# Optimization experiments

Measured on AMD Instinct MI355X. Metric: run time of the kernel, lower is better.

## Reference

```python
import jax, jax.numpy as jnp
import numpy as np

B, D, PRE, NXT, J, K, A = 1000, 8, 98, 2048, 32, 64, 5

def setup_inputs() -> dict:
    key = jax.random.key(0)
    ks = jax.random.split(key, 20)
    s = 0.05  # weight scale to keep activations sane
    inp = {
        'x': jax.random.normal(ks[0], (B, D * PRE), jnp.float32),
        'W1': jax.random.normal(ks[1], (D, NXT, PRE), jnp.float32) * s,
        'b1': jax.random.normal(ks[2], (D, NXT), jnp.float32) * s,
        'Wc': jax.random.normal(ks[3], (D, J, NXT), jnp.float32) * s,
        'bc': jax.random.normal(ks[4], (D, J), jnp.float32) * s,
        'cut_layer_bias': jax.random.normal(ks[5], (J,), jnp.float32) * s,
        'b_mat': jax.random.normal(ks[6], (D, J), jnp.float32) * s,
        'h_mat': jax.random.normal(ks[7], (D, K, A), jnp.float32),
        'a_mat': jax.random.normal(ks[8], (J, A), jnp.float32) * s,
        'noise': jax.random.normal(ks[9], (J, A), jnp.float32),  # tau2 = 1.0
        'W3': jax.random.normal(ks[10], (98, J), jnp.float32) * s,
        'b3': jax.random.normal(ks[11], (98,), jnp.float32) * s,
        'W4': jax.random.normal(ks[12], (49, 98), jnp.float32) * s,
        'b4': jax.random.normal(ks[13], (49,), jnp.float32) * s,
        'Wo': jax.random.normal(ks[14], (10, 49), jnp.float32) * s,
        'bo': jax.random.normal(ks[15], (10,), jnp.float32) * s,
    }
    # one-hot subcarrier allocation: each symbol j assigned exactly one subcarrier k
    assign = jax.random.randint(ks[16], (J,), 0, K)
    inp['indicator'] = jax.nn.one_hot(assign, K, dtype=jnp.float32)
    return inp


def reference(x, W1, b1, Wc, bc, cut_layer_bias, b_mat, h_mat, a_mat, indicator,
              noise, W3, b3, W4, b4, Wo, bo):
    b = x.shape[0]
    xs = x.reshape(b, D, PRE)                                   # split across devices
    sub = jax.nn.relu(jnp.einsum('bdi,doi->bdo', xs, W1) + b1)  # [B,D,NXT]
    # online cross-device mean/var via .item() in torch => stats are non-differentiable scalars
    m = jnp.mean(sub, axis=(0, 2))                              # per-device mean [D]
    v = jnp.mean((sub - m[None, :, None]) ** 2, axis=(0, 2))    # per-device var  [D]
    gm = jax.lax.stop_gradient(jnp.mean(m))
    gv = jax.lax.stop_gradient(jnp.mean(v))
    norm = (sub - gm) / jnp.sqrt(gv + 1e-6)
    dso = jnp.einsum('bdo,djo->bdj', norm, Wc) + bc             # device-side outputs [B,D,J]
    # channel: gather assigned subcarrier per symbol, combine with receive beamformers a_j
    h_sel = jnp.einsum('jk,nkd->njd', indicator, h_mat)         # [D,J,A]
    h_vec = jnp.einsum('njd,jd->nj', h_sel, a_mat)              # [D,J]
    received = jnp.einsum('bnj,nj->bj', dso * b_mat[None], h_vec)  # [B,J]
    received = received + jnp.sum(a_mat * noise, axis=1)[None, :]  # scaled noise per symbol
    h = jax.nn.relu(received + cut_layer_bias)
    h = jax.nn.relu(h @ W3.T + b3)
    h = jax.nn.relu(h @ W4.T + b4)
    return jax.nn.log_softmax(h @ Wo.T + bo, axis=1)
```

## Files before the change

kernel.cpp:

```cpp
#include <hip/hip_runtime.h>
#include <math.h>

#define B_ 1000
#define D_ 8
#define PRE_ 98
#define NXT_ 2048
#define J_ 32
#define K_ 64
#define A_ 5

typedef __attribute__((ext_vector_type(8))) __bf16 bf16x8;
typedef __attribute__((ext_vector_type(4))) float f32x4;
typedef __attribute__((ext_vector_type(16))) float f32x16;
typedef __attribute__((ext_vector_type(8))) unsigned short us8;

__device__ __forceinline__ unsigned cvtpk(float lo, float hi) {
  unsigned r;
  asm("v_cvt_pk_bf16_f32 %0, %1, %2" : "=v"(r) : "v"(lo), "v"(hi));
  return r;
}

__device__ __forceinline__ void gload16(const void* g, void* l) {
  __builtin_amdgcn_global_load_lds(
      (const __attribute__((address_space(1))) void*)g,
      (__attribute__((address_space(3))) void*)l, 16, 0, 0);
}

union bfu { unsigned u[4]; bf16x8 v; };


__global__ __launch_bounds__(256) void kcvt(
    const float* __restrict__ x, const float* __restrict__ W1,
    const float* __restrict__ b1, const float* __restrict__ Wc,
    const float* __restrict__ h_mat, const float* __restrict__ a_mat,
    const float* __restrict__ noise, const float* __restrict__ indicator,
    unsigned short* __restrict__ w1a, unsigned short* __restrict__ xa,
    unsigned short* __restrict__ wca, float* __restrict__ wcp,
    float* __restrict__ hvec, float* __restrict__ nz) {
  __shared__ float sbuf[32 * 257];
  __shared__ float extra[32];
  __shared__ float ws2[32][9];

  const int bid = blockIdx.x, tid = threadIdx.x;

  if (bid < 512) {
    const int d = bid & 7, og = bid >> 3;
    const float* base = W1 + (size_t)3136 * (d * 64 + og);
    for (int idx = tid; idx < 784; idx += 256) {
      float4 v4 = ((const float4*)base)[idx];
      int p = idx * 4;
      const float vv[4] = {v4.x, v4.y, v4.z, v4.w};
#pragma unroll
      for (int e = 0; e < 4; ++e) {
        int pp = p + e;
        int r = pp / 98, k = pp - r * 98;
        sbuf[r * 99 + k] = vv[e];
      }
    }
    if (tid < 32) extra[tid] = b1[d * NXT_ + og * 32 + tid];
    __syncthreads();
    unsigned short* dst = w1a + (size_t)((d * 64 + og) * 7) * 512;
#pragma unroll
    for (int q = 0; q < 2; ++q) {
      int s = tid + q * 256;
      if (s < 448) {
        int ks = s >> 6, l = s & 63;
        int r = l & 31, k0 = ks * 16 + (l >> 5) * 8;
        const float* row = sbuf + r * 99;
        bfu v;
#pragma unroll
        for (int p = 0; p < 4; ++p) {
          int k = k0 + 2 * p;
          float f0 = (k < 98) ? row[k] : ((k == 98) ? extra[r] : 0.0f);
          float f1 = (k + 1 < 98) ? row[k + 1] : ((k + 1 == 98) ? extra[r] : 0.0f);
          v.u[p] = cvtpk(f0, f1);
        }
        *(bf16x8*)(dst + (size_t)s * 8) = v.v;
      }
    }
  } else if (bid < 768) {
    const int b2 = bid - 512;
    const int d = b2 & 7, bg = b2 >> 3;
    for (int idx = tid; idx < 1568; idx += 256) {
      int r = idx / 49, c = idx - r * 49;
      int gb = bg * 32 + r;
      float2 v2 = make_float2(0.0f, 0.0f);
      if (gb < B_)
        v2 = *(const float2*)(x + (size_t)gb * (D_ * PRE_) + d * PRE_ + 2 * c);
      sbuf[r * 99 + 2 * c] = v2.x;
      sbuf[r * 99 + 2 * c + 1] = v2.y;
    }
    __syncthreads();
    unsigned short* dst = xa + (size_t)((d * 32 + bg) * 7) * 512;
#pragma unroll
    for (int q = 0; q < 2; ++q) {
      int s = tid + q * 256;
      if (s < 448) {
        int ks = s >> 6, l = s & 63;
        int r = l & 31, k0 = ks * 16 + (l >> 5) * 8;
        bool valid = (bg * 32 + r) < B_;
        const float* row = sbuf + r * 99;
        bfu v;
#pragma unroll
        for (int p = 0; p < 4; ++p) {
          int k = k0 + 2 * p;
          float f0 = 0.0f, f1 = 0.0f;
          if (valid) {
            f0 = (k < 98) ? row[k] : ((k == 98) ? 1.0f : 0.0f);
            f1 = (k + 1 < 98) ? row[k + 1] : ((k + 1 == 98) ? 1.0f : 0.0f);
          }
          v.u[p] = cvtpk(f0, f1);
        }
        *(bf16x8*)(dst + (size_t)s * 8) = v.v;
      }
    }
  } else if (bid < 832) {
    const int b3 = bid - 768;
    const int d = b3 & 7, oq = b3 >> 3;
    for (int idx = tid; idx < 2048; idx += 256) {
      int j = idx >> 6, c = idx & 63;
      float4 v4 = *(const float4*)(Wc + ((size_t)d * J_ + j) * NXT_ +
                                   oq * 256 + 4 * c);
      float* p = sbuf + j * 257 + 4 * c;
      p[0] = v4.x;
      p[1] = v4.y;
      p[2] = v4.z;
      p[3] = v4.w;
    }
    __syncthreads();
    unsigned short* dst = wca + (size_t)((d * 64 + oq * 8) * 2) * 512;
#pragma unroll
    for (int q = 0; q < 4; ++q) {
      int s = tid + q * 256;
      int ogl = s >> 7, t2 = (s >> 6) & 1, l = s & 63;
      int j = l & 31;
      int ol = ogl * 32 + t2 * 16 + (l >> 5) * 8;
      const float* row = sbuf + j * 257 + ol;
      bfu v;
#pragma unroll
      for (int p = 0; p < 4; ++p) v.u[p] = cvtpk(row[2 * p], row[2 * p + 1]);
      *(bf16x8*)(dst + (size_t)s * 8) = v.v;
    }
    {
      int j = tid >> 3, seg = tid & 7;
      const float* row = sbuf + j * 257 + seg * 32;
      float sacc = 0.0f;
#pragma unroll
      for (int i = 0; i < 32; ++i) sacc += row[i];
      ws2[j][seg] = sacc;
    }
    __syncthreads();
    if (tid < 32) {
      float t = 0.0f;
#pragma unroll
      for (int g = 0; g < 8; ++g) t += ws2[tid][g];
      wcp[((size_t)d * 32 + tid) * 8 + oq] = t;
    }
  } else {
    int dd = tid >> 5, j = tid & 31;
    float hs[A_] = {0, 0, 0, 0, 0};
    for (int k = 0; k < K_; ++k) {
      float indv = indicator[j * K_ + k];
      if (indv != 0.0f) {
        const float* hp = h_mat + ((size_t)dd * K_ + k) * A_;
#pragma unroll
        for (int a = 0; a < A_; ++a) hs[a] = fmaf(indv, hp[a], hs[a]);
      }
    }
    float hv = 0.0f;
#pragma unroll
    for (int a = 0; a < A_; ++a) hv = fmaf(hs[a], a_mat[j * A_ + a], hv);
    hvec[tid] = hv;
    if (tid < J_) {
      float nzv = 0.0f;
#pragma unroll
      for (int a = 0; a < A_; ++a)
        nzv = fmaf(a_mat[tid * A_ + a], noise[tid * A_ + a], nzv);
      nz[tid] = nzv;
    }
  }
}

__global__ __launch_bounds__(512, 4) void k1(
    const unsigned short* __restrict__ w1a,
    const unsigned short* __restrict__ xa,
    const unsigned short* __restrict__ wca, float* __restrict__ S1part,
    float* __restrict__ spsum, float* __restrict__ spsq) {
  extern __shared__ __align__(16) char smem[];

  const int id = blockIdx.x;
  const int d = id & 7;
  const int rest = id >> 3;
  const int bt = rest & 15, oc = rest >> 4;
  const int tid = threadIdx.x;
  const int w = tid >> 6, lane = tid & 63;
  const int bh = w >> 2, q = w & 3;
  const int l31 = lane & 31, hi = lane >> 5;
  const bool lo_half = (hi == 0);

  {
    const unsigned short* w1src =
        w1a + ((size_t)d * 448 + oc * 56) * 512 + lane * 8;
    const unsigned short* wcsrc =
        wca + ((size_t)d * 128 + oc * 16) * 512 + lane * 8;
#pragma unroll
    for (int c = 0; c < 9; ++c) {
      int f = w * 9 + c;
      const unsigned short* src = (f < 56) ? (w1src + (size_t)f * 512)
                                           : (wcsrc + (size_t)(f - 56) * 512);
      gload16(src, smem + (size_t)f * 1024);
    }
  }

  bf16x8 xf[7];
  {
    const unsigned short* xb =
        xa + (size_t)((d * 32 + bt * 2 + bh) * 7) * 512 + lane * 8;
#pragma unroll
    for (int ks = 0; ks < 7; ++ks) xf[ks] = *(const bf16x8*)(xb + ks * 512);
  }
  __syncthreads();

  f32x16 acc2 = {};
  float lsum = 0.0f, lsq = 0.0f;

#pragma unroll
  for (int i2 = 0; i2 < 2; ++i2) {
    const int ogl = q * 2 + i2;
    const char* ab = smem + (size_t)(ogl * 7) * 1024 + lane * 16;
    const char* wb = smem + (size_t)(56 + ogl * 2) * 1024 + lane * 16;
    bf16x8 wc0 = *(const bf16x8*)(wb);
    bf16x8 wc1 = *(const bf16x8*)(wb + 1024);

    f32x16 acc = {};
#pragma unroll
    for (int ks = 0; ks < 7; ++ks) {
      bf16x8 a = *(const bf16x8*)(ab + (size_t)ks * 1024);
      acc = __builtin_amdgcn_mfma_f32_32x32x16_bf16(a, xf[ks], acc, 0, 0, 0);
    }

    float v[16];
#pragma unroll
    for (int r = 0; r < 16; ++r) {
      v[r] = fmaxf(acc[r], 0.0f);
      lsum += v[r];
      lsq = fmaf(v[r], v[r], lsq);
    }
#pragma unroll
    for (int t = 0; t < 2; ++t) {
      unsigned A0 = cvtpk(v[8 * t + 0], v[8 * t + 1]);
      unsigned A1 = cvtpk(v[8 * t + 2], v[8 * t + 3]);
      unsigned B0 = cvtpk(v[8 * t + 4], v[8 * t + 5]);
      unsigned B1 = cvtpk(v[8 * t + 6], v[8 * t + 7]);
      unsigned sA0 = __shfl_xor(A0, 32);
      unsigned sA1 = __shfl_xor(A1, 32);
      unsigned sB0 = __shfl_xor(B0, 32);
      unsigned sB1 = __shfl_xor(B1, 32);
      bfu f;
      f.u[0] = lo_half ? A0 : sB0;
      f.u[1] = lo_half ? A1 : sB1;
      f.u[2] = lo_half ? sA0 : B0;
      f.u[3] = lo_half ? sA1 : B1;
      acc2 = __builtin_amdgcn_mfma_f32_32x32x16_bf16(t == 0 ? wc0 : wc1, f.v,
                                                     acc2, 0, 0, 0);
    }
  }

  __syncthreads();
  float* redf = (float*)smem;
  {
#pragma unroll
    for (int r = 0; r < 16; ++r) {
      int j = (r & 3) + 8 * (r >> 2) + 4 * hi;
      redf[(bh * 4 + q) * 1056 + l31 * 33 + j] = acc2[r];
    }
  }
  __syncthreads();

  {
    const int half = tid >> 8;
    const int row = (tid >> 3) & 31;
    const int j0 = (tid & 7) * 4;
    f32x4 s;
#pragma unroll
    for (int e = 0; e < 4; ++e) {
      float acc_ = 0.0f;
#pragma unroll
      for (int ww = 0; ww < 4; ++ww)
        acc_ += redf[(half * 4 + ww) * 1056 + row * 33 + j0 + e];
      s[e] = acc_;
    }
    const int b = (bt * 2 + half) * 32 + row;
    *(f32x4*)(S1part + (((size_t)oc * 1024 + b) * 8 + d) * 32 + j0) = s;
  }

#pragma unroll
  for (int off = 32; off; off >>= 1) {
    lsum += __shfl_down(lsum, off);
    lsq += __shfl_down(lsq, off);
  }
  if (lane == 0) {
    spsum[id * 8 + w] = lsum;
    spsq[id * 8 + w] = lsq;
  }
}

#define W3S 33
#define W4S 99

__global__ __launch_bounds__(256) void kB(
    const float* __restrict__ S1part, const float* __restrict__ spsum,
    const float* __restrict__ spsq, const float* __restrict__ wcp,
    const float* __restrict__ hvec, const float* __restrict__ nz,
    const float* __restrict__ bc, const float* __restrict__ b_mat,
    const float* __restrict__ cutb, const float* __restrict__ W3,
    const float* __restrict__ b3, const float* __restrict__ W4,
    const float* __restrict__ b4, const float* __restrict__ Wo,
    const float* __restrict__ bo, float* __restrict__ out) {
  __shared__ float W3l[98 * W3S];
  __shared__ float W4l[49 * W4S];
  __shared__ float Wol[490];
  __shared__ float b3l[98], b4l[49], bol[10];
  __shared__ float cutl[32], coefl[256], konstl[32], wcs[256];
  __shared__ float psum[8][33], psq[8][33];
  __shared__ float mvals[8], vvals[8];
  __shared__ float sh_gm, sh_inv;
  __shared__ float offs[D_][J_];
  __shared__ float h1[4][32];
  __shared__ float h2[4][100];
  __shared__ float h3[4][52];
  __shared__ float lg[4][10];
  __shared__ float lsel[4];

  const int tid = threadIdx.x;

  for (int idx = tid; idx < 784; idx += 256) {
    float4 v4 = ((const float4*)W3)[idx];
    int p = idx * 4;
    const float vv[4] = {v4.x, v4.y, v4.z, v4.w};
#pragma unroll
    for (int e = 0; e < 4; ++e) {
      int pp = p + e;
      W3l[(pp >> 5) * W3S + (pp & 31)] = vv[e];
    }
  }
  for (int idx = tid; idx < 2401; idx += 256) {
    float2 v2 = ((const float2*)W4)[idx];
    int p = idx * 2;
    int o = p / 98, k = p - o * 98;
    W4l[o * W4S + k] = v2.x;
    W4l[o * W4S + k + 1] = v2.y;
  }
  if (tid < 245) {
    float2 v2 = ((const float2*)Wo)[tid];
    Wol[2 * tid] = v2.x;
    Wol[2 * tid + 1] = v2.y;
  }
  if (tid < 49) {
    float2 v2 = ((const float2*)b3)[tid];
    b3l[2 * tid] = v2.x;
    b3l[2 * tid + 1] = v2.y;
    b4l[tid] = b4[tid];
  }
  if (tid < 10) bol[tid] = bo[tid];
  if (tid < 32) cutl[tid] = cutb[tid];

  {
    const float4* p = (const float4*)(wcp + (size_t)tid * 8);
    float4 a = p[0], b = p[1];
    wcs[tid] = a.x + a.y + a.z + a.w + b.x + b.y + b.z + b.w;
  }

  {
    int dd = tid >> 5, i = tid & 31;
    float s = 0.0f, q = 0.0f;
#pragma unroll
    for (int m = 0; m < 4; ++m) {
      int rest = i + m * 32;
      int base = (rest * 8 + dd) * 8;
#pragma unroll
      for (int ww = 0; ww < 8; ++ww) {
        s += spsum[base + ww];
        q += spsq[base + ww];
      }
    }
    psum[dd][i] = s;
    psq[dd][i] = q;
  }
  __syncthreads();
  if (tid < 8) {
    float s = 0.0f, q = 0.0f;
#pragma unroll
    for (int i = 0; i < 32; ++i) {
      s += psum[tid][i];
      q += psq[tid][i];
    }
    const float inv_cnt = 1.0f / ((float)B_ * (float)NXT_);
    float m = s * inv_cnt;
    mvals[tid] = m;
    vvals[tid] = q * inv_cnt - m * m;
  }
  __syncthreads();
  if (tid == 0) {
    float gm = 0.0f, gv = 0.0f;
    for (int dd = 0; dd < 8; ++dd) {
      gm += mvals[dd];
      gv += vvals[dd];
    }
    gm *= 0.125f;
    gv *= 0.125f;
    sh_gm = gm;
    sh_inv = 1.0f / sqrtf(gv + 1e-6f);
  }
  __syncthreads();
  {
    int dd = tid >> 5, j = tid & 31;
    float c = b_mat[dd * J_ + j] * hvec[tid];
    coefl[tid] = c * sh_inv;
    offs[dd][j] = c * (bc[dd * J_ + j] - sh_gm * wcs[tid] * sh_inv);
  }
  __syncthreads();
  if (tid < J_) {
    float s = nz[tid];
#pragma unroll
    for (int dd = 0; dd < D_; ++dd) s += offs[dd][tid];
    konstl[tid] = s;
  }
  __syncthreads();

  const int row = tid >> 6, lane = tid & 63;
  const int b = blockIdx.x * 4 + row;

  if (lane < 32) {
    float rsum = konstl[lane];
#pragma unroll
    for (int dd = 0; dd < D_; ++dd) {
      float s = 0.0f;
#pragma unroll
      for (int p = 0; p < 8; ++p)
        s += S1part[(((size_t)p * 1024 + b) * 8 + dd) * 32 + lane];
      rsum = fmaf(coefl[dd * J_ + lane], s, rsum);
    }
    h1[row][lane] = fmaxf(rsum + cutl[lane], 0.0f);
  }
  __syncthreads();

  for (int o = lane; o < 98; o += 64) {
    float a = b3l[o];
#pragma unroll
    for (int j = 0; j < 32; ++j) a = fmaf(h1[row][j], W3l[o * W3S + j], a);
    h2[row][o] = fmaxf(a, 0.0f);
  }
  __syncthreads();

  if (lane < 49) {
    float a = b4l[lane];
    for (int k = 0; k < 98; ++k)
      a = fmaf(h2[row][k], W4l[lane * W4S + k], a);
    h3[row][lane] = fmaxf(a, 0.0f);
  }
  __syncthreads();

  if (lane < 10) {
    float a = bol[lane];
#pragma unroll
    for (int k = 0; k < 49; ++k) a = fmaf(h3[row][k], Wol[lane * 49 + k], a);
    lg[row][lane] = a;
  }
  __syncthreads();
  if (lane == 0) {
    float mx = lg[row][0];
    for (int i = 1; i < 10; ++i) mx = fmaxf(mx, lg[row][i]);
    float se = 0.0f;
    for (int i = 0; i < 10; ++i) se += expf(lg[row][i] - mx);
    lsel[row] = mx + logf(se);
  }
  __syncthreads();
  if (lane < 10) out[(size_t)b * 10 + lane] = lg[row][lane] - lsel[row];
}

extern "C" void kernel_launch(void* const* d_in, const int* in_sizes, int n_in,
                              void* d_out, int out_size, void* d_ws,
                              size_t ws_size, hipStream_t stream) {
  const float* x = (const float*)d_in[0];
  const float* W1 = (const float*)d_in[1];
  const float* b1 = (const float*)d_in[2];
  const float* Wc = (const float*)d_in[3];
  const float* bc = (const float*)d_in[4];
  const float* cutb = (const float*)d_in[5];
  const float* bmat = (const float*)d_in[6];
  const float* hmat = (const float*)d_in[7];
  const float* amat = (const float*)d_in[8];
  const float* noise = (const float*)d_in[9];
  const float* W3 = (const float*)d_in[10];
  const float* b3 = (const float*)d_in[11];
  const float* W4 = (const float*)d_in[12];
  const float* b4 = (const float*)d_in[13];
  const float* Wo = (const float*)d_in[14];
  const float* bo = (const float*)d_in[15];
  const float* ind = (const float*)d_in[16];

  float* ws = (float*)d_ws;
  float* S1part = ws;
  unsigned short* w1a = (unsigned short*)(ws + 2097152);
  unsigned short* xa = (unsigned short*)(ws + 2555904);
  unsigned short* wca = (unsigned short*)(ws + 2785280);
  float* spsum = ws + 3047424;
  float* spsq = ws + 3055616;
  float* wcp = ws + 3063808;
  float* hvec = ws + 3065856;
  float* nz = ws + 3066112;

  kcvt<<<833, 256, 0, stream>>>(x, W1, b1, Wc, hmat, amat, noise, ind, w1a,
                                xa, wca, wcp, hvec, nz);
  k1<<<1024, 512, 73728, stream>>>(w1a, xa, wca, S1part, spsum, spsq);
  kB<<<250, 256, 0, stream>>>(S1part, spsum, spsq, wcp, hvec, nz, bc, bmat,
                              cutb, W3, b3, W4, b4, Wo, bo, (float*)d_out);
}
```

Measured before the change: 45.56 us.

## Stage x in LDS and stream weights from global, halving k1 grid

k1 now stages the two x batch tiles in LDS and has each wave read its W1 and Wc fragments straight from global memory. Each wave computes two output groups against both batch halves, reusing each weight fragment for two MFMAs. The grid shrinks from 1024 to 512 blocks, so there are half as many S1part partial slices and stat partials, and kB's reduction loops are shortened to match. The aim is to cut partial-sum write and reduce traffic and the LDS weight staging. The cost is more direct global or L2 weight loads with no LDS prefetch, which could expose load latency.

New measurement: 50.61 us. +11.1%, slower.

```diff
diff --git a/kernel.cpp b/kernel.cpp
--- a/kernel.cpp
+++ b/kernel.cpp
@@ -194,75 +194,75 @@
   const int bt = rest & 15, oc = rest >> 4;
   const int tid = threadIdx.x;
   const int w = tid >> 6, lane = tid & 63;
-  const int bh = w >> 2, q = w & 3;
   const int l31 = lane & 31, hi = lane >> 5;
   const bool lo_half = (hi == 0);
 
-  {
-    const unsigned short* w1src =
-        w1a + ((size_t)d * 448 + oc * 56) * 512 + lane * 8;
-    const unsigned short* wcsrc =
-        wca + ((size_t)d * 128 + oc * 16) * 512 + lane * 8;
-#pragma unroll
-    for (int c = 0; c < 9; ++c) {
-      int f = w * 9 + c;
-      const unsigned short* src = (f < 56) ? (w1src + (size_t)f * 512)
-                                           : (wcsrc + (size_t)(f - 56) * 512);
+#pragma unroll
+  for (int c = 0; c < 2; ++c) {
+    int f = w * 2 + c;
+    if (f < 14) {
+      int bgl = f / 7, ks = f - bgl * 7;
+      const unsigned short* src =
+          xa + (size_t)((d * 32 + bt * 2 + bgl) * 7 + ks) * 512 + lane * 8;
       gload16(src, smem + (size_t)f * 1024);
     }
   }
-
-  bf16x8 xf[7];
-  {
-    const unsigned short* xb =
-        xa + (size_t)((d * 32 + bt * 2 + bh) * 7) * 512 + lane * 8;
-#pragma unroll
-    for (int ks = 0; ks < 7; ++ks) xf[ks] = *(const bf16x8*)(xb + ks * 512);
-  }
-  __syncthreads();
-
-  f32x16 acc2 = {};
+  __syncthreads();
+
+  f32x16 acc2a = {}, acc2b = {};
   float lsum = 0.0f, lsq = 0.0f;
 
-#pragma unroll
-  for (int i2 = 0; i2 < 2; ++i2) {
-    const int ogl = q * 2 + i2;
-    const char* ab = smem + (size_t)(ogl * 7) * 1024 + lane * 16;
-    const char* wb = smem + (size_t)(56 + ogl * 2) * 1024 + lane * 16;
+  for (int og2 = 0; og2 < 2; ++og2) {
+    const int og = oc * 16 + w * 2 + og2;
+    const unsigned short* ab =
+        w1a + (size_t)((d * 64 + og) * 7) * 512 + lane * 8;
+    const unsigned short* wb =
+        wca + (size_t)((d * 64 + og) * 2) * 512 + lane * 8;
     bf16x8 wc0 = *(const bf16x8*)(wb);
-    bf16x8 wc1 = *(const bf16x8*)(wb + 1024);
-
-    f32x16 acc = {};
+    bf16x8 wc1 = *(const bf16x8*)(wb + 512);
+
+    f32x16 acca = {}, accb = {};
 #pragma unroll
     for (int ks = 0; ks < 7; ++ks) {
-      bf16x8 a = *(const bf16x8*)(ab + (size_t)ks * 1024);
-      acc = __builtin_amdgcn_mfma_f32_32x32x16_bf16(a, xf[ks], acc, 0, 0, 0);
-    }
-
-    float v[16];
-#pragma unroll
-    for (int r = 0; r < 16; ++r) {
-      v[r] = fmaxf(acc[r], 0.0f);
-      lsum += v[r];
-      lsq = fmaf(v[r], v[r], lsq);
-    }
-#pragma unroll
-    for (int t = 0; t < 2; ++t) {
-      unsigned A0 = cvtpk(v[8 * t + 0], v[8 * t + 1]);
-      unsigned A1 = cvtpk(v[8 * t + 2], v[8 * t + 3]);
-      unsigned B0 = cvtpk(v[8 * t + 4], v[8 * t + 5]);
-      unsigned B1 = cvtpk(v[8 * t + 6], v[8 * t + 7]);
-      unsigned sA0 = __shfl_xor(A0, 32);
-      unsigned sA1 = __shfl_xor(A1, 32);
-      unsigned sB0 = __shfl_xor(B0, 32);
-      unsigned sB1 = __shfl_xor(B1, 32);
-      bfu f;
-      f.u[0] = lo_half ? A0 : sB0;
-      f.u[1] = lo_half ? A1 : sB1;
-      f.u[2] = lo_half ? sA0 : B0;
-      f.u[3] = lo_half ? sA1 : B1;
-      acc2 = __builtin_amdgcn_mfma_f32_32x32x16_bf16(t == 0 ? wc0 : wc1, f.v,
-                                                     acc2, 0, 0, 0);
+      bf16x8 a = *(const bf16x8*)(ab + (size_t)ks * 512);
+      bf16x8 x0 = *(const bf16x8*)(smem + (size_t)ks * 1024 + lane * 16);
+      bf16x8 x1 = *(const bf16x8*)(smem + (size_t)(7 + ks) * 1024 + lane * 16);
+      acca = __builtin_amdgcn_mfma_f32_32x32x16_bf16(a, x0, acca, 0, 0, 0);
+      accb = __builtin_amdgcn_mfma_f32_32x32x16_bf16(a, x1, accb, 0, 0, 0);
+    }
+
+#pragma unroll
+    for (int q = 0; q < 2; ++q) {
+      const f32x16& src = q ? accb : acca;
+      float v[16];
+#pragma unroll
+      for (int r = 0; r < 16; ++r) {
+        v[r] = fmaxf(src[r], 0.0f);
+        lsum += v[r];
+        lsq = fmaf(v[r], v[r], lsq);
+      }
+#pragma unroll
+      for (int t = 0; t < 2; ++t) {
+        unsigned A0 = cvtpk(v[8 * t + 0], v[8 * t + 1]);
+        unsigned A1 = cvtpk(v[8 * t + 2], v[8 * t + 3]);
+        unsigned B0 = cvtpk(v[8 * t + 4], v[8 * t + 5]);
+        unsigned B1 = cvtpk(v[8 * t + 6], v[8 * t + 7]);
+        unsigned sA0 = __shfl_xor(A0, 32);
+        unsigned sA1 = __shfl_xor(A1, 32);
+        unsigned sB0 = __shfl_xor(B0, 32);
+        unsigned sB1 = __shfl_xor(B1, 32);
+        bfu f;
+        f.u[0] = lo_half ? A0 : sB0;
+        f.u[1] = lo_half ? A1 : sB1;
+        f.u[2] = lo_half ? sA0 : B0;
+        f.u[3] = lo_half ? sA1 : B1;
+        if (q == 0)
+          acc2a = __builtin_amdgcn_mfma_f32_32x32x16_bf16(t == 0 ? wc0 : wc1,
+                                                          f.v, acc2a, 0, 0, 0);
+        else
+          acc2b = __builtin_amdgcn_mfma_f32_32x32x16_bf16(t == 0 ? wc0 : wc1,
+                                                          f.v, acc2b, 0, 0, 0);
+      }
     }
   }
 
@@ -272,7 +272,8 @@
 #pragma unroll
     for (int r = 0; r < 16; ++r) {
       int j = (r & 3) + 8 * (r >> 2) + 4 * hi;
-      redf[(bh * 4 + q) * 1056 + l31 * 33 + j] = acc2[r];
+      redf[(w * 2 + 0) * 1056 + l31 * 33 + j] = acc2a[r];
+      redf[(w * 2 + 1) * 1056 + l31 * 33 + j] = acc2b[r];
     }
   }
   __syncthreads();
@@ -286,8 +287,8 @@
     for (int e = 0; e < 4; ++e) {
       float acc_ = 0.0f;
 #pragma unroll
-      for (int ww = 0; ww < 4; ++ww)
-        acc_ += redf[(half * 4 + ww) * 1056 + row * 33 + j0 + e];
+      for (int ww = 0; ww < 8; ++ww)
+        acc_ += redf[(ww * 2 + half) * 1056 + row * 33 + j0 + e];
       s[e] = acc_;
     }
     const int b = (bt * 2 + half) * 32 + row;
@@ -375,7 +376,7 @@
     int dd = tid >> 5, i = tid & 31;
     float s = 0.0f, q = 0.0f;
 #pragma unroll
-    for (int m = 0; m < 4; ++m) {
+    for (int m = 0; m < 2; ++m) {
       int rest = i + m * 32;
       int base = (rest * 8 + dd) * 8;
 #pragma unroll
@@ -437,7 +438,7 @@
     for (int dd = 0; dd < D_; ++dd) {
       float s = 0.0f;
 #pragma unroll
-      for (int p = 0; p < 8; ++p)
+      for (int p = 0; p < 4; ++p)
         s += S1part[(((size_t)p * 1024 + b) * 8 + dd) * 32 + lane];
       rsum = fmaf(coefl[dd * J_ + lane], s, rsum);
     }
@@ -502,18 +503,18 @@
 
   float* ws = (float*)d_ws;
   float* S1part = ws;
-  unsigned short* w1a = (unsigned short*)(ws + 2097152);
-  unsigned short* xa = (unsigned short*)(ws + 2555904);
-  unsigned short* wca = (unsigned short*)(ws + 2785280);
-  float* spsum = ws + 3047424;
-  float* spsq = ws + 3055616;
-  float* wcp = ws + 3063808;
-  float* hvec = ws + 3065856;
-  float* nz = ws + 3066112;
+  unsigned short* w1a = (unsigned short*)(ws + 1048576);
+  unsigned short* xa = (unsigned short*)(ws + 1966080);
+  unsigned short* wca = (unsigned short*)(ws + 2424832);
+  float* spsum = ws + 2686976;
+  float* spsq = ws + 2691072;
+  float* wcp = ws + 2695168;
+  float* hvec = ws + 2697216;
+  float* nz = ws + 2697472;
 
   kcvt<<<833, 256, 0, stream>>>(x, W1, b1, Wc, hmat, amat, noise, ind, w1a,
                                 xa, wca, wcp, hvec, nz);
-  k1<<<1024, 512, 73728, stream>>>(w1a, xa, wca, S1part, spsum, spsq);
+  k1<<<512, 512, 67584, stream>>>(w1a, xa, wca, S1part, spsum, spsq);
   kB<<<250, 256, 0, stream>>>(S1part, spsum, spsq, wcp, hvec, nz, bc, bmat,
                               cutb, W3, b3, W4, b4, Wo, bo, (float*)d_out);
 }
```
